# Kernel optimization log

Measured on AMD Instinct MI355X. Metric: run time of the kernel, lower is better.

The kernel has to match this reference:

```python
import jax, jax.numpy as jnp
import numpy as np

N_NODES = 100000
N_EDGES = 1600000
D_IN = 64
D_OUT = 64
CLAMP = -10000.0  # scatter_'max' post-clamp threshold from the source


def setup_inputs() -> dict:
    key = jax.random.key(0)
    k1, k2, k3, k4, k5 = jax.random.split(key, 5)
    n_feat = jax.random.normal(k1, (N_NODES, D_IN), dtype=jnp.float32)
    src = jax.random.randint(k2, (N_EDGES,), 0, N_NODES, dtype=jnp.int64)
    dst = jax.random.randint(k3, (N_EDGES,), 0, N_NODES, dtype=jnp.int64)
    W = jax.random.normal(k4, (2 * D_IN, D_OUT), dtype=jnp.float32) / np.sqrt(2 * D_IN)
    b = jax.random.normal(k5, (D_OUT,), dtype=jnp.float32) * 0.01
    return {"n_feat": n_feat, "src": src, "dst": dst, "W": W, "b": b}


def reference(n_feat, src, dst, W, b):
    # gather endpoint features and form relative messages: [E, d]
    diff = n_feat[src] - n_feat[dst]
    # scatter-max aggregate onto destination nodes: [N, d]
    agg = jax.ops.segment_max(diff, dst, num_segments=n_feat.shape[0])
    # torch_scatter fills empty slots with lowest value; source clamps out<-10000 to 0
    agg = jnp.where(agg < CLAMP, 0.0, agg)
    # concat original + aggregated, then MLP = Linear + ReLU: [N, 2d] @ [2d, out]
    h = jnp.concatenate([n_feat, agg], axis=1)
    return jax.nn.relu(h @ W + b)
```

## Files before the change

kernel.cpp:

```cpp
#include <hip/hip_runtime.h>
#include <hip/hip_bf16.h>

#define D 64
#define CLAMP_V -10000.0f
#define SBSHIFT 9
#define SBN 512
#define MAXSB 256
#define HCHUNK 4096
#define SCHUNK 4096
#define NPW 8

typedef __bf16 bf16x4 __attribute__((ext_vector_type(4)));
typedef __bf16 bf16x8 __attribute__((ext_vector_type(8)));
typedef float floatx4 __attribute__((ext_vector_type(4)));
typedef unsigned short u16x2 __attribute__((ext_vector_type(2)));
typedef short s16x2 __attribute__((ext_vector_type(2)));

__device__ __forceinline__ unsigned pkmax(unsigned a, unsigned b) {
    u16x2 r = __builtin_elementwise_max(__builtin_bit_cast(u16x2, a),
                                        __builtin_bit_cast(u16x2, b));
    return __builtin_bit_cast(unsigned, r);
}
__device__ __forceinline__ uint4 pkmax4(uint4 a, uint4 b) {
    uint4 r;
    r.x = pkmax(a.x, b.x); r.y = pkmax(a.y, b.y);
    r.z = pkmax(a.z, b.z); r.w = pkmax(a.w, b.w);
    return r;
}
__device__ __forceinline__ unsigned pk_ord_encode(unsigned g) {
    s16x2 t = __builtin_bit_cast(s16x2, g) >> 15;
    unsigned m = __builtin_bit_cast(unsigned, t) & 0x7FFF7FFFu;
    return g ^ (m | 0x80008000u);
}
__device__ __forceinline__ unsigned pk_ord_decode(unsigned e) {
    s16x2 t = __builtin_bit_cast(s16x2, e) >> 15;
    unsigned m = (~__builtin_bit_cast(unsigned, t)) & 0x7FFF7FFFu;
    return e ^ (m | 0x80008000u);
}
__device__ __forceinline__ unsigned seg_finish(unsigned enc, unsigned xr) {
    unsigned raw = pk_ord_decode(enc);
    float v0 = __uint_as_float(raw << 16);
    float v1 = __uint_as_float(raw & 0xFFFF0000u);
    float x0 = __uint_as_float(xr << 16);
    float x1 = __uint_as_float(xr & 0xFFFF0000u);
    float r0 = v0 - x0; r0 = (r0 >= CLAMP_V) ? r0 : 0.0f;
    float r1 = v1 - x1; r1 = (r1 >= CLAMP_V) ? r1 : 0.0f;
    __bf16 b0 = (__bf16)r0, b1 = (__bf16)r1;
    return ((unsigned)__builtin_bit_cast(unsigned short, b1) << 16)
         |  (unsigned)__builtin_bit_cast(unsigned short, b0);
}

__global__ __launch_bounds__(256) void prep_kernel(
        const float* __restrict__ nf, __bf16* __restrict__ nf16,
        unsigned* __restrict__ nfenc, int n4,
        const int* __restrict__ dst, unsigned* __restrict__ ghist,
        int nE, int nbSB,
        const float* __restrict__ W, __bf16* __restrict__ wfrag,
        int histBlocks, int wBlock) {
    __shared__ unsigned h[MAXSB];
    int blk = blockIdx.x, t = threadIdx.x;
    int i = blk * 256 + t;
    if (i < n4) {
        float4 v = ((const float4*)nf)[i];
        __bf16 b0 = (__bf16)v.x, b1 = (__bf16)v.y;
        __bf16 b2 = (__bf16)v.z, b3 = (__bf16)v.w;
        bf16x4 o = { b0, b1, b2, b3 };
        ((bf16x4*)nf16)[i] = o;
        unsigned d0 = ((unsigned)__builtin_bit_cast(unsigned short, b1) << 16)
                    |  (unsigned)__builtin_bit_cast(unsigned short, b0);
        unsigned d1 = ((unsigned)__builtin_bit_cast(unsigned short, b3) << 16)
                    |  (unsigned)__builtin_bit_cast(unsigned short, b2);
        uint2 e; e.x = pk_ord_encode(d0); e.y = pk_ord_encode(d1);
        ((uint2*)nfenc)[i] = e;
    }
    if (blk < histBlocks) {
        if (t < MAXSB) h[t] = 0;
        __syncthreads();
        int e0 = blk * HCHUNK;
        int ec = nE - e0; if (ec > HCHUNK) ec = HCHUNK;
        for (int k = t; k < ec; k += 256) atomicAdd(&h[dst[e0 + k] >> SBSHIFT], 1u);
        __syncthreads();
        if (t < (unsigned)nbSB && h[t]) atomicAdd(&ghist[t], h[t]);
    }
    if (blk == wBlock) {
        for (int idx = t; idx < 2 * D * D; idx += 256) {
            int k = idx >> 6, n = idx & 63;
            int ks = k >> 5, r = k & 31, quad = r >> 3, j = r & 7;
            int c = n >> 4, l16 = n & 15;
            int fidx = (((ks * 4 + c) * 64) + quad * 16 + l16) * 8 + j;
            wfrag[fidx] = (__bf16)W[idx];
        }
    }
}

__global__ __launch_bounds__(256) void scan_sb(
        const unsigned* __restrict__ ghist, unsigned* __restrict__ base,
        unsigned* __restrict__ cursor, int nbSB) {
    __shared__ unsigned ts[256];
    int t = threadIdx.x;
    unsigned v = (t < nbSB) ? ghist[t] : 0u;
    ts[t] = v; __syncthreads();
    for (int off = 1; off < 256; off <<= 1) {
        unsigned x = (t >= off) ? ts[t - off] : 0u;
        __syncthreads();
        ts[t] += x;
        __syncthreads();
    }
    if (t < nbSB) {
        unsigned ex = ts[t] - v;
        base[t] = ex; cursor[t] = ex;
        if (t == nbSB - 1) base[nbSB] = ts[t];
    }
}

__global__ __launch_bounds__(256) void sb_scatter(
        const int* __restrict__ src, const int* __restrict__ dst,
        unsigned* __restrict__ cursor, unsigned* __restrict__ packed,
        int nE, int nbSB) {
    __shared__ unsigned cop[MAXSB];
    __shared__ unsigned short lb16[MAXSB];
    __shared__ unsigned gbase[MAXSB];
    __shared__ unsigned payload[SCHUNK];
    __shared__ unsigned char sbid[SCHUNK];
    __shared__ unsigned ts[256];
    int t = threadIdx.x;
    int e0 = blockIdx.x * SCHUNK;
    int ec = nE - e0; if (ec > SCHUNK) ec = SCHUNK;

    if (t < MAXSB) cop[t] = 0;
    __syncthreads();
    for (int i = t; i < ec; i += 256)
        atomicAdd(&cop[dst[e0 + i] >> SBSHIFT], 1u);
    __syncthreads();
    unsigned c = (t < nbSB) ? (cop[t] & 0xFFFFu) : 0u;
    ts[t] = c; __syncthreads();
    for (int o = 1; o < 256; o <<= 1) {
        unsigned x = (t >= o) ? ts[t - o] : 0u;
        __syncthreads();
        ts[t] += x;
        __syncthreads();
    }
    if (t < nbSB) {
        lb16[t] = (unsigned short)(ts[t] - c);
        if (c) gbase[t] = atomicAdd(&cursor[t], c);
    }
    __syncthreads();
    for (int i = t; i < ec; i += 256) {
        int e = e0 + i;
        int d = dst[e];
        int b = d >> SBSHIFT;
        unsigned p = atomicAdd(&cop[b], 0x10000u) >> 16;
        unsigned pos = (unsigned)lb16[b] + p;
        payload[pos] = ((unsigned)(d & (SBN - 1)) << 17) | (unsigned)src[e];
        sbid[pos] = (unsigned char)b;
    }
    __syncthreads();
    for (int i = t; i < ec; i += 256) {
        unsigned b = sbid[i];
        packed[gbase[b] + ((unsigned)i - (unsigned)lb16[b])] = payload[i];
    }
}

__global__ __launch_bounds__(256) void sb_sort(
        const unsigned* __restrict__ packed1, const unsigned* __restrict__ base,
        unsigned* __restrict__ packed2, unsigned* __restrict__ nodestart,
        int nN) {
    __shared__ unsigned cnt[SBN];
    __shared__ unsigned ts[256];
    int sb = blockIdx.x, t = threadIdx.x;
    unsigned beg = base[sb], end = base[sb + 1];
    cnt[2 * t] = 0; cnt[2 * t + 1] = 0;
    __syncthreads();
    for (unsigned i = beg + t; i < end; i += 256)
        atomicAdd(&cnt[packed1[i] >> 17], 1u);
    __syncthreads();
    unsigned a = cnt[2 * t], b = cnt[2 * t + 1], s = a + b;
    ts[t] = s; __syncthreads();
    for (int o = 1; o < 256; o <<= 1) {
        unsigned x = (t >= o) ? ts[t - o] : 0u;
        __syncthreads();
        ts[t] += x;
        __syncthreads();
    }
    unsigned ex = ts[t] - s;
    cnt[2 * t] = ex; cnt[2 * t + 1] = ex + a;
    int n0 = sb * SBN;
    if (n0 + 2 * t     <= nN) nodestart[n0 + 2 * t]     = beg + ex;
    if (n0 + 2 * t + 1 <= nN) nodestart[n0 + 2 * t + 1] = beg + ex + a;
    __syncthreads();
    for (unsigned i = beg + t; i < end; i += 256) {
        unsigned e = packed1[i];
        unsigned p = atomicAdd(&cnt[e >> 17], 1u);
        packed2[beg + p] = e & 0x1FFFFu;
    }
}

__global__ __launch_bounds__(256) void seg_direct(
        const uint4* __restrict__ enc4,
        const uint4* __restrict__ nfu4,
        const unsigned* __restrict__ packed2,
        const unsigned* __restrict__ nodestart,
        uint4* __restrict__ agg4,
        int nN) {
    int t = threadIdx.x;
    int wv = t >> 6, ln = t & 63;
    int grp = ln >> 3;
    int col = ln & 7;
    int n0 = blockIdx.x * (4 * NPW) + wv * NPW;
    #pragma unroll 1
    for (int k = 0; k < NPW; ++k) {
        int n = n0 + k;
        if (n >= nN) break;
        unsigned rb = nodestart[n], re = nodestart[n + 1];
        uint4 a0 = {0,0,0,0}, a1 = {0,0,0,0}, a2 = {0,0,0,0}, a3 = {0,0,0,0};
        for (unsigned c = rb; c < re; c += 64) {
            unsigned idx = c + (unsigned)ln;
            unsigned pe = (idx < re) ? packed2[idx] : 0u;
            int lim = (int)(re - c); if (lim > 64) lim = 64;
            int j = 0;
            for (; j + 32 <= lim; j += 32) {
                unsigned e0 = __shfl(pe, j      + grp, 64);
                unsigned e1 = __shfl(pe, j + 8  + grp, 64);
                unsigned e2 = __shfl(pe, j + 16 + grp, 64);
                unsigned e3 = __shfl(pe, j + 24 + grp, 64);
                uint4 g0 = enc4[(size_t)e0 * 8 + col];
                uint4 g1 = enc4[(size_t)e1 * 8 + col];
                uint4 g2 = enc4[(size_t)e2 * 8 + col];
                uint4 g3 = enc4[(size_t)e3 * 8 + col];
                a0 = pkmax4(a0, g0);
                a1 = pkmax4(a1, g1);
                a2 = pkmax4(a2, g2);
                a3 = pkmax4(a3, g3);
            }
            for (; j < lim; j += 8) {
                int jj = j + grp; if (jj >= lim) jj = lim - 1;
                unsigned e = __shfl(pe, jj, 64);
                uint4 g = enc4[(size_t)e * 8 + col];
                a0 = pkmax4(a0, g);
            }
        }
        uint4 m = pkmax4(pkmax4(a0, a1), pkmax4(a2, a3));
        #pragma unroll
        for (int dd = 8; dd < 64; dd <<= 1) {
            uint4 o;
            o.x = __shfl_xor(m.x, dd, 64);
            o.y = __shfl_xor(m.y, dd, 64);
            o.z = __shfl_xor(m.z, dd, 64);
            o.w = __shfl_xor(m.w, dd, 64);
            m = pkmax4(m, o);
        }
        if (ln < 8) {
            uint4 xr = nfu4[(size_t)n * 8 + ln];
            uint4 o;
            o.x = seg_finish(m.x, xr.x);
            o.y = seg_finish(m.y, xr.y);
            o.z = seg_finish(m.z, xr.z);
            o.w = seg_finish(m.w, xr.w);
            agg4[(size_t)n * 8 + ln] = o;
        }
    }
}

__global__ __launch_bounds__(256) void node_mlp_mfma(
        const __bf16* __restrict__ nf16,
        const __bf16* __restrict__ agg16,
        float* __restrict__ out,
        const __bf16* __restrict__ wfrag,
        const float* __restrict__ bias,
        int nTiles, int nN) {
    int lane = threadIdx.x & 63;
    int quad = lane >> 4;
    int l16  = lane & 15;
    int waveGlobal = blockIdx.x * 4 + (threadIdx.x >> 6);
    int nWaves = gridDim.x * 4;

    bf16x8 bfrag[4][4];
    #pragma unroll
    for (int c = 0; c < 4; ++c)
        #pragma unroll
        for (int ks = 0; ks < 4; ++ks)
            bfrag[c][ks] = *(const bf16x8*)(wfrag + ((size_t)((ks * 4 + c) * 64 + lane)) * 8);
    float bv[4];
    #pragma unroll
    for (int c = 0; c < 4; ++c) bv[c] = bias[c * 16 + l16];

    for (int t = waveGlobal; t < nTiles; t += nWaves) {
        int n0 = t * 16;
        int rowA = n0 + l16;
        if (rowA >= nN) rowA = nN - 1;
        const __bf16* nfr = nf16  + (size_t)rowA * D;
        const __bf16* agr = agg16 + (size_t)rowA * D;

        floatx4 acc[4] = {{0,0,0,0},{0,0,0,0},{0,0,0,0},{0,0,0,0}};
        #pragma unroll
        for (int ks = 0; ks < 4; ++ks) {
            const __bf16* p = (ks < 2) ? (nfr + ks * 32 + quad * 8)
                                       : (agr + (ks - 2) * 32 + quad * 8);
            bf16x8 a = *(const bf16x8*)p;
            #pragma unroll
            for (int c = 0; c < 4; ++c)
                acc[c] = __builtin_amdgcn_mfma_f32_16x16x32_bf16(
                             a, bfrag[c][ks], acc[c], 0, 0, 0);
        }
        #pragma unroll
        for (int r = 0; r < 4; ++r) {
            int row = n0 + quad * 4 + r;
            if (row < nN) {
                #pragma unroll
                for (int c = 0; c < 4; ++c) {
                    float vv = acc[c][r] + bv[c];
                    out[(size_t)row * D + c * 16 + l16] = fmaxf(vv, 0.0f);
                }
            }
        }
    }
}

extern "C" void kernel_launch(void* const* d_in, const int* in_sizes, int n_in,
                              void* d_out, int out_size, void* d_ws, size_t ws_size,
                              hipStream_t stream) {
    const float* nf  = (const float*)d_in[0];
    const int*   src = (const int*)d_in[1];
    const int*   dst = (const int*)d_in[2];
    const float* W   = (const float*)d_in[3];
    const float* b   = (const float*)d_in[4];
    float* out = (float*)d_out;

    int nN = in_sizes[0] / D;
    int nE = in_sizes[1];
    int nbSB = (nN + SBN - 1) / SBN;

    char* wsb = (char*)d_ws;
    size_t nfB  = (((size_t)nN * D * 2) + 255) & ~(size_t)255;
    size_t pkB  = (((size_t)nE * 4)     + 255) & ~(size_t)255;
    __bf16*   nf16   = (__bf16*)wsb;
    __bf16*   agg16  = (__bf16*)(wsb + nfB);
    unsigned* packed1 = (unsigned*)(wsb + 2 * nfB);
    unsigned* ghist  = (unsigned*)(wsb + 2 * nfB + pkB);
    unsigned* base   = (unsigned*)(wsb + 2 * nfB + pkB + 4 * MAXSB);
    unsigned* cursor = (unsigned*)(wsb + 2 * nfB + pkB + 4 * MAXSB + 4 * (MAXSB + 2));
    __bf16*   wfrag  = (__bf16*)(wsb + 2 * nfB + pkB + 4 * MAXSB + 8 * (MAXSB + 2));
    unsigned* nodestart = (unsigned*)(wsb + 2 * nfB + pkB + 4 * MAXSB
                                      + 8 * (MAXSB + 2) + 32768);
    unsigned* packed2 = (unsigned*)d_out;
    unsigned* nfenc   = (unsigned*)((char*)d_out + pkB);

    hipMemsetAsync(ghist, 0, (size_t)nbSB * 4, stream);

    int n4 = nN * D / 4;
    int convBlocks = (n4 + 255) / 256;
    int histBlocks = (nE + HCHUNK - 1) / HCHUNK;
    int gridPrep = convBlocks > histBlocks ? convBlocks : histBlocks;
    prep_kernel<<<gridPrep, 256, 0, stream>>>(nf, nf16, nfenc, n4, dst, ghist,
                                              nE, nbSB, W, wfrag,
                                              histBlocks, gridPrep - 1);

    scan_sb<<<1, 256, 0, stream>>>(ghist, base, cursor, nbSB);

    int nbS = (nE + SCHUNK - 1) / SCHUNK;
    sb_scatter<<<nbS, 256, 0, stream>>>(src, dst, cursor, packed1, nE, nbSB);

    sb_sort<<<nbSB, 256, 0, stream>>>(packed1, base, packed2, nodestart, nN);

    int segBlocks = (nN + 4 * NPW - 1) / (4 * NPW);
    seg_direct<<<segBlocks, 256, 0, stream>>>(
        (const uint4*)nfenc, (const uint4*)nf16, packed2, nodestart,
        (uint4*)agg16, nN);

    int nTiles = (nN + 15) / 16;
    node_mlp_mfma<<<768, 256, 0, stream>>>(nf16, agg16, out, wfrag, b, nTiles, nN);
}
```

Measured before the change: 206.3 us.

## Assign one 8-lane group per node in segment-max instead of one wave

The segment-max kernel now maps each node to an 8-lane group, so each wave handles 8 nodes at once. Previously a whole wave looped over its nodes one at a time and used shuffles plus a cross-lane reduction. Each lane now reads the edge indices itself and accumulates over that node's edges sequentially. This removes the per-chunk shuffles, the xor reduction and most idle lanes at average degree 16, at the cost of divergence when node degrees differ within a wave.

```diff
diff --git a/kernel.cpp b/kernel.cpp
--- a/kernel.cpp
+++ b/kernel.cpp
@@ -8,7 +8,6 @@
 #define MAXSB 256
 #define HCHUNK 4096
 #define SCHUNK 4096
-#define NPW 8
 
 typedef __bf16 bf16x4 __attribute__((ext_vector_type(4)));
 typedef __bf16 bf16x8 __attribute__((ext_vector_type(8)));
@@ -203,62 +202,42 @@
         uint4* __restrict__ agg4,
         int nN) {
     int t = threadIdx.x;
-    int wv = t >> 6, ln = t & 63;
+    int ln = t & 63;
     int grp = ln >> 3;
     int col = ln & 7;
-    int n0 = blockIdx.x * (4 * NPW) + wv * NPW;
-    #pragma unroll 1
-    for (int k = 0; k < NPW; ++k) {
-        int n = n0 + k;
-        if (n >= nN) break;
-        unsigned rb = nodestart[n], re = nodestart[n + 1];
-        uint4 a0 = {0,0,0,0}, a1 = {0,0,0,0}, a2 = {0,0,0,0}, a3 = {0,0,0,0};
-        for (unsigned c = rb; c < re; c += 64) {
-            unsigned idx = c + (unsigned)ln;
-            unsigned pe = (idx < re) ? packed2[idx] : 0u;
-            int lim = (int)(re - c); if (lim > 64) lim = 64;
-            int j = 0;
-            for (; j + 32 <= lim; j += 32) {
-                unsigned e0 = __shfl(pe, j      + grp, 64);
-                unsigned e1 = __shfl(pe, j + 8  + grp, 64);
-                unsigned e2 = __shfl(pe, j + 16 + grp, 64);
-                unsigned e3 = __shfl(pe, j + 24 + grp, 64);
-                uint4 g0 = enc4[(size_t)e0 * 8 + col];
-                uint4 g1 = enc4[(size_t)e1 * 8 + col];
-                uint4 g2 = enc4[(size_t)e2 * 8 + col];
-                uint4 g3 = enc4[(size_t)e3 * 8 + col];
-                a0 = pkmax4(a0, g0);
-                a1 = pkmax4(a1, g1);
-                a2 = pkmax4(a2, g2);
-                a3 = pkmax4(a3, g3);
-            }
-            for (; j < lim; j += 8) {
-                int jj = j + grp; if (jj >= lim) jj = lim - 1;
-                unsigned e = __shfl(pe, jj, 64);
-                uint4 g = enc4[(size_t)e * 8 + col];
-                a0 = pkmax4(a0, g);
-            }
-        }
-        uint4 m = pkmax4(pkmax4(a0, a1), pkmax4(a2, a3));
-        #pragma unroll
-        for (int dd = 8; dd < 64; dd <<= 1) {
-            uint4 o;
-            o.x = __shfl_xor(m.x, dd, 64);
-            o.y = __shfl_xor(m.y, dd, 64);
-            o.z = __shfl_xor(m.z, dd, 64);
-            o.w = __shfl_xor(m.w, dd, 64);
-            m = pkmax4(m, o);
-        }
-        if (ln < 8) {
-            uint4 xr = nfu4[(size_t)n * 8 + ln];
-            uint4 o;
-            o.x = seg_finish(m.x, xr.x);
-            o.y = seg_finish(m.y, xr.y);
-            o.z = seg_finish(m.z, xr.z);
-            o.w = seg_finish(m.w, xr.w);
-            agg4[(size_t)n * 8 + ln] = o;
-        }
-    }
+    int n = blockIdx.x * 32 + (t >> 6) * 8 + grp;
+    if (n >= nN) return;
+    unsigned rb = nodestart[n], re = nodestart[n + 1];
+    unsigned deg = re - rb;
+    const uint4* ec = enc4 + col;
+    uint4 a0 = {0,0,0,0}, a1 = {0,0,0,0}, a2 = {0,0,0,0}, a3 = {0,0,0,0};
+    unsigned i = 0;
+    for (; i + 4 <= deg; i += 4) {
+        unsigned e0 = packed2[rb + i];
+        unsigned e1 = packed2[rb + i + 1];
+        unsigned e2 = packed2[rb + i + 2];
+        unsigned e3 = packed2[rb + i + 3];
+        uint4 g0 = ec[(size_t)e0 * 8];
+        uint4 g1 = ec[(size_t)e1 * 8];
+        uint4 g2 = ec[(size_t)e2 * 8];
+        uint4 g3 = ec[(size_t)e3 * 8];
+        a0 = pkmax4(a0, g0);
+        a1 = pkmax4(a1, g1);
+        a2 = pkmax4(a2, g2);
+        a3 = pkmax4(a3, g3);
+    }
+    for (; i < deg; ++i) {
+        unsigned e0 = packed2[rb + i];
+        a0 = pkmax4(a0, ec[(size_t)e0 * 8]);
+    }
+    uint4 m = pkmax4(pkmax4(a0, a1), pkmax4(a2, a3));
+    uint4 xr = nfu4[(size_t)n * 8 + col];
+    uint4 o;
+    o.x = seg_finish(m.x, xr.x);
+    o.y = seg_finish(m.y, xr.y);
+    o.z = seg_finish(m.z, xr.z);
+    o.w = seg_finish(m.w, xr.w);
+    agg4[(size_t)n * 8 + col] = o;
 }
 
 __global__ __launch_bounds__(256) void node_mlp_mfma(
@@ -362,7 +341,7 @@
 
     sb_sort<<<nbSB, 256, 0, stream>>>(packed1, base, packed2, nodestart, nN);
 
-    int segBlocks = (nN + 4 * NPW - 1) / (4 * NPW);
+    int segBlocks = (nN + 31) / 32;
     seg_direct<<<segBlocks, 256, 0, stream>>>(
         (const uint4*)nfenc, (const uint4*)nf16, packed2, nodestart,
         (uint4*)agg16, nN);
```

Measured after the change: 195.8 us. -5.1%, faster.
